# Optimization experiments

Hardware: AMD Instinct MI355X
Metric: run time of the kernel (lower is better)

The kernel has to match this reference:

```python
import jax, jax.numpy as jnp
import numpy as np

EPS = 1e-12  # F.normalize default eps (norm clamped to at least eps)


def setup_inputs() -> dict:
    key = jax.random.key(0)
    k1, k2, k3, k4 = jax.random.split(key, 4)
    B, Cin, Cout, H, W = 8, 128, 32, 256, 256
    x = jax.random.normal(k1, (B, Cin, H, W), dtype=jnp.float32)
    qk = jax.random.normal(k2, (B, 2 * Cout, H, W), dtype=jnp.float32)
    # 1x1 conv params (PyTorch Conv2d default init scale ~ 1/sqrt(fan_in))
    w_v = jax.random.normal(k3, (Cout, Cin), dtype=jnp.float32) / np.sqrt(Cin)
    b_v = jax.random.normal(k4, (Cout,), dtype=jnp.float32) / np.sqrt(Cin)
    temperature = jnp.ones((1, 1, 1), dtype=jnp.float32)
    return {"x": x, "qk": qk, "w_v": w_v, "b_v": b_v, "temperature": temperature}


def reference(x, qk, w_v, b_v, temperature):
    B, Cin, H, W = x.shape
    Co = w_v.shape[0]
    N = H * W
    # 1x1 conv == channel GEMM
    v = jnp.einsum('bchw,oc->bohw', x, w_v) + b_v[None, :, None, None]
    # split qk: k = first Co channels, q = last Co channels; head=1
    q = qk[:, Co:].reshape(B, 1, Co, N)
    k = qk[:, :Co].reshape(B, 1, Co, N)
    v = v.reshape(B, 1, Co, N)
    # L2-normalize over spatial dim (F.normalize: divide by max(norm, eps))
    q = q / jnp.maximum(jnp.linalg.norm(q, axis=-1, keepdims=True), EPS)
    k = k / jnp.maximum(jnp.linalg.norm(k, axis=-1, keepdims=True), EPS)
    # channel-wise (transposed) attention: [B,1,Co,Co]
    attn = jnp.einsum('bhcn,bhdn->bhcd', q, k) * temperature
    attn = jax.nn.softmax(attn, axis=-1)
    out = jnp.einsum('bhcd,bhdn->bhcn', attn, v)  # [B,1,Co,N]
    return out
```

## Files before the change

kernel.cpp:

```cpp
#include <hip/hip_runtime.h>
#include <hip/hip_bf16.h>
#include <math.h>

#define NB    8
#define CIN   128
#define CO    32
#define CH    64
#define NN    65536
#define CHUNKS 128
#define GXB   32
#define SPW   (NN/CHUNKS)
#define SLABS (SPW/16)

typedef __attribute__((ext_vector_type(8))) short bf16x8;
typedef __attribute__((ext_vector_type(16))) float f32x16;

__device__ __forceinline__ short f2bf(float f) {
    union { __hip_bfloat16 h; short s; } u;
    u.h = __float2bfloat16(f);
    return u.s;
}
__device__ __forceinline__ float bf2f(short s) {
    union { __hip_bfloat16 h; short s; } u;
    u.s = s;
    return __bfloat162float(u.h);
}

__global__ __launch_bounds__(256) void gram_kernel(const float* __restrict__ qk,
                                                   float* __restrict__ part,
                                                   float* __restrict__ partsq) {
    const int b = blockIdx.y;
    const int w = threadIdx.x >> 6;
    const int l = threadIdx.x & 63;
    const int chunk = blockIdx.x * 4 + w;
    const int c = l & 31;
    const int half = l >> 5;

    const float* qrow = qk + (size_t)b * CH * NN + (size_t)(CO + c) * NN
                        + (size_t)chunk * SPW + half * 8;
    const float* krow = qk + (size_t)b * CH * NN + (size_t)c * NN
                        + (size_t)chunk * SPW + half * 8;

    f32x16 acc = {};
    float sqq = 0.f, sqk = 0.f;

#pragma unroll 4
    for (int s = 0; s < SLABS; ++s) {
        float4 q0 = *(const float4*)(qrow + s * 16);
        float4 q1 = *(const float4*)(qrow + s * 16 + 4);
        float4 k0 = *(const float4*)(krow + s * 16);
        float4 k1 = *(const float4*)(krow + s * 16 + 4);

        float qf[8] = {q0.x, q0.y, q0.z, q0.w, q1.x, q1.y, q1.z, q1.w};
        float kf[8] = {k0.x, k0.y, k0.z, k0.w, k1.x, k1.y, k1.z, k1.w};

        bf16x8 ah, al, bh, bl;
#pragma unroll
        for (int j = 0; j < 8; ++j) {
            short hq = f2bf(qf[j]);
            ah[j] = hq;
            al[j] = f2bf(qf[j] - bf2f(hq));
            short hk = f2bf(kf[j]);
            bh[j] = hk;
            bl[j] = f2bf(kf[j] - bf2f(hk));
            sqq = fmaf(qf[j], qf[j], sqq);
            sqk = fmaf(kf[j], kf[j], sqk);
        }
        acc = __builtin_amdgcn_mfma_f32_32x32x16_bf16(ah, bh, acc, 0, 0, 0);
        acc = __builtin_amdgcn_mfma_f32_32x32x16_bf16(ah, bl, acc, 0, 0, 0);
        acc = __builtin_amdgcn_mfma_f32_32x32x16_bf16(al, bh, acc, 0, 0, 0);
    }

    sqq += __shfl_xor(sqq, 32);
    sqk += __shfl_xor(sqk, 32);
    if (half == 0) {
        float* psq = partsq + ((size_t)b * CHUNKS + chunk) * 64;
        psq[c] = sqk;
        psq[CO + c] = sqq;
    }

    float* pp = part + ((size_t)b * CHUNKS + chunk) * 1024;
#pragma unroll
    for (int r = 0; r < 16; ++r) {
        int row = (r & 3) + 8 * (r >> 2) + 4 * half;
        pp[row * 32 + c] = acc[r];
    }
}

__global__ __launch_bounds__(128) void reduce_kernel(const float* __restrict__ part,
                                                     const float* __restrict__ partsq,
                                                     float* __restrict__ Sred) {
    const int b = blockIdx.y;
    const int v = blockIdx.x * 64 + (threadIdx.x >> 1);
    const int h = threadIdx.x & 1;
    float s = 0.f;
    if (v < 1024) {
        const float* p = part + (size_t)b * CHUNKS * 1024 + v;
        for (int ch = h * (CHUNKS / 2); ch < (h + 1) * (CHUNKS / 2); ++ch)
            s += p[(size_t)ch * 1024];
    } else {
        const float* p = partsq + (size_t)b * CHUNKS * 64 + (v - 1024);
        for (int ch = h * (CHUNKS / 2); ch < (h + 1) * (CHUNKS / 2); ++ch)
            s += p[(size_t)ch * 64];
    }
    s += __shfl_xor(s, 1);
    if (h == 0) Sred[b * 1088 + v] = s;
}

__global__ __launch_bounds__(256) void attn_kernel(const float* __restrict__ Sred,
                                                   const float* __restrict__ w_v,
                                                   const float* __restrict__ b_v,
                                                   const float* __restrict__ temp,
                                                   float* __restrict__ Weff,
                                                   float* __restrict__ beff) {
    __shared__ float sS[1024];
    __shared__ float snorm[64];
    __shared__ float sA[1024];
    const int t = threadIdx.x;
    const int b = blockIdx.x;

    for (int i = t; i < 1024; i += 256) sS[i] = Sred[b * 1088 + i];
    if (t < 64) snorm[t] = fmaxf(sqrtf(Sred[b * 1088 + 1024 + t]), 1e-12f);
    __syncthreads();

    if (t < 32) {
        const float T = temp[0];
        const float qn = snorm[32 + t];
        float m = -1e30f;
        for (int d = 0; d < 32; ++d)
            m = fmaxf(m, sS[t * 32 + d] / (qn * snorm[d]) * T);
        float sum = 0.f;
        for (int d = 0; d < 32; ++d)
            sum += expf(sS[t * 32 + d] / (qn * snorm[d]) * T - m);
        const float inv = 1.f / sum;
        for (int d = 0; d < 32; ++d)
            sA[t * 32 + d] = expf(sS[t * 32 + d] / (qn * snorm[d]) * T - m) * inv;
    }
    __syncthreads();

    for (int idx = t; idx < CO * CIN; idx += 256) {
        int cc = idx >> 7;
        int ci = idx & 127;
        float s = 0.f;
#pragma unroll
        for (int d = 0; d < 32; ++d) s += sA[cc * 32 + d] * w_v[d * CIN + ci];
        Weff[(size_t)b * CO * CIN + idx] = s;
    }
    if (t < 32) {
        float s = 0.f;
#pragma unroll
        for (int d = 0; d < 32; ++d) s += sA[t * 32 + d] * b_v[d];
        beff[b * CO + t] = s;
    }
}

__global__ __launch_bounds__(256) void out_kernel(const float* __restrict__ x,
                                                  const float* __restrict__ Weff,
                                                  const float* __restrict__ beff,
                                                  float* __restrict__ out) {
    const int b = blockIdx.y;
    const int n0 = blockIdx.x * 512 + threadIdx.x * 2;
    const float* xb = x + (size_t)b * CIN * NN + n0;
    const float* Wb = Weff + (size_t)b * CO * CIN;
    const float* bb = beff + b * CO;

    float a0[CO], a1[CO];
#pragma unroll
    for (int o = 0; o < CO; ++o) { a0[o] = bb[o]; a1[o] = bb[o]; }

#pragma unroll 4
    for (int ci = 0; ci < CIN; ++ci) {
        float2 xv = *(const float2*)(xb + (size_t)ci * NN);
#pragma unroll
        for (int o = 0; o < CO; ++o) {
            float wv = Wb[o * CIN + ci];
            a0[o] = fmaf(wv, xv.x, a0[o]);
            a1[o] = fmaf(wv, xv.y, a1[o]);
        }
    }

    float* ob = out + (size_t)b * CO * NN + n0;
#pragma unroll
    for (int o = 0; o < CO; ++o) {
        float2 r;
        r.x = a0[o];
        r.y = a1[o];
        *(float2*)(ob + (size_t)o * NN) = r;
    }
}

extern "C" void kernel_launch(void* const* d_in, const int* in_sizes, int n_in,
                              void* d_out, int out_size, void* d_ws, size_t ws_size,
                              hipStream_t stream) {
    const float* x    = (const float*)d_in[0];
    const float* qk   = (const float*)d_in[1];
    const float* w_v  = (const float*)d_in[2];
    const float* b_v  = (const float*)d_in[3];
    const float* temp = (const float*)d_in[4];
    float* out = (float*)d_out;

    float* part   = (float*)d_ws;
    float* partsq = part + (size_t)NB * CHUNKS * 1024;
    float* Sred   = partsq + (size_t)NB * CHUNKS * 64;
    float* Weff   = Sred + (size_t)NB * 1088;
    float* beff   = Weff + (size_t)NB * CO * CIN;

    gram_kernel<<<dim3(GXB, NB), 256, 0, stream>>>(qk, part, partsq);
    reduce_kernel<<<dim3(17, NB), 128, 0, stream>>>(part, partsq, Sred);
    attn_kernel<<<dim3(NB), 256, 0, stream>>>(Sred, w_v, b_v, temp, Weff, beff);
    out_kernel<<<dim3(NN / 512, NB), 256, 0, stream>>>(x, Weff, beff, out);
}
```

Baseline: 119.9 us.

## Widen gram grid with in-block reduction, fuse reduce into finalize, vectorize weight loads

The gram kernel now launches 128 chunks per batch instead of 32. Each block's four waves split a chunk and sum their partial Gram matrices in shared memory before writing one result. The separate reduce kernel is folded into the attention/finalize kernel, which removes one launch but runs the 128-chunk reduction inside only 8 blocks. The output kernel reads the effective weights as float4 over four input channels, which cuts the number of scalar weight loads.

```diff
diff --git a/kernel.cpp b/kernel.cpp
--- a/kernel.cpp
+++ b/kernel.cpp
@@ -8,8 +8,8 @@
 #define CH    64
 #define NN    65536
 #define CHUNKS 128
-#define GXB   32
-#define SPW   (NN/CHUNKS)
+#define SPC   (NN/CHUNKS)
+#define SPW   (SPC/4)
 #define SLABS (SPW/16)
 
 typedef __attribute__((ext_vector_type(8))) short bf16x8;
@@ -29,22 +29,24 @@
 __global__ __launch_bounds__(256) void gram_kernel(const float* __restrict__ qk,
                                                    float* __restrict__ part,
                                                    float* __restrict__ partsq) {
+    __shared__ float red[4 * 1024];
+    __shared__ float red2[4 * 64];
+
     const int b = blockIdx.y;
+    const int chunk = blockIdx.x;
     const int w = threadIdx.x >> 6;
     const int l = threadIdx.x & 63;
-    const int chunk = blockIdx.x * 4 + w;
     const int c = l & 31;
     const int half = l >> 5;
 
-    const float* qrow = qk + (size_t)b * CH * NN + (size_t)(CO + c) * NN
-                        + (size_t)chunk * SPW + half * 8;
-    const float* krow = qk + (size_t)b * CH * NN + (size_t)c * NN
-                        + (size_t)chunk * SPW + half * 8;
+    const size_t colbase = (size_t)chunk * SPC + (size_t)w * SPW + half * 8;
+    const float* qrow = qk + (size_t)b * CH * NN + (size_t)(CO + c) * NN + colbase;
+    const float* krow = qk + (size_t)b * CH * NN + (size_t)c * NN + colbase;
 
     f32x16 acc = {};
     float sqq = 0.f, sqk = 0.f;
 
-#pragma unroll 4
+#pragma unroll 2
     for (int s = 0; s < SLABS; ++s) {
         float4 q0 = *(const float4*)(qrow + s * 16);
         float4 q1 = *(const float4*)(qrow + s * 16 + 4);
@@ -74,53 +76,59 @@
     sqq += __shfl_xor(sqq, 32);
     sqk += __shfl_xor(sqk, 32);
     if (half == 0) {
-        float* psq = partsq + ((size_t)b * CHUNKS + chunk) * 64;
-        psq[c] = sqk;
-        psq[CO + c] = sqq;
-    }
-
-    float* pp = part + ((size_t)b * CHUNKS + chunk) * 1024;
+        red2[w * 64 + c] = sqk;
+        red2[w * 64 + 32 + c] = sqq;
+    }
+
 #pragma unroll
     for (int r = 0; r < 16; ++r) {
         int row = (r & 3) + 8 * (r >> 2) + 4 * half;
-        pp[row * 32 + c] = acc[r];
-    }
-}
-
-__global__ __launch_bounds__(128) void reduce_kernel(const float* __restrict__ part,
-                                                     const float* __restrict__ partsq,
-                                                     float* __restrict__ Sred) {
-    const int b = blockIdx.y;
-    const int v = blockIdx.x * 64 + (threadIdx.x >> 1);
-    const int h = threadIdx.x & 1;
-    float s = 0.f;
-    if (v < 1024) {
-        const float* p = part + (size_t)b * CHUNKS * 1024 + v;
-        for (int ch = h * (CHUNKS / 2); ch < (h + 1) * (CHUNKS / 2); ++ch)
-            s += p[(size_t)ch * 1024];
-    } else {
-        const float* p = partsq + (size_t)b * CHUNKS * 64 + (v - 1024);
-        for (int ch = h * (CHUNKS / 2); ch < (h + 1) * (CHUNKS / 2); ++ch)
-            s += p[(size_t)ch * 64];
-    }
-    s += __shfl_xor(s, 1);
-    if (h == 0) Sred[b * 1088 + v] = s;
-}
-
-__global__ __launch_bounds__(256) void attn_kernel(const float* __restrict__ Sred,
-                                                   const float* __restrict__ w_v,
-                                                   const float* __restrict__ b_v,
-                                                   const float* __restrict__ temp,
-                                                   float* __restrict__ Weff,
-                                                   float* __restrict__ beff) {
+        red[w * 1024 + row * 32 + c] = acc[r];
+    }
+    __syncthreads();
+
+    float* pp = part + ((size_t)b * CHUNKS + chunk) * 1024;
+#pragma unroll
+    for (int k = 0; k < 4; ++k) {
+        int idx = threadIdx.x + k * 256;
+        pp[idx] = red[idx] + red[1024 + idx] + red[2048 + idx] + red[3072 + idx];
+    }
+    if (threadIdx.x < 64) {
+        partsq[((size_t)b * CHUNKS + chunk) * 64 + threadIdx.x] =
+            red2[threadIdx.x] + red2[64 + threadIdx.x] +
+            red2[128 + threadIdx.x] + red2[192 + threadIdx.x];
+    }
+}
+
+__global__ __launch_bounds__(256) void finalize_kernel(const float* __restrict__ part,
+                                                       const float* __restrict__ partsq,
+                                                       const float* __restrict__ w_v,
+                                                       const float* __restrict__ b_v,
+                                                       const float* __restrict__ temp,
+                                                       float* __restrict__ Weff,
+                                                       float* __restrict__ beff) {
     __shared__ float sS[1024];
     __shared__ float snorm[64];
     __shared__ float sA[1024];
     const int t = threadIdx.x;
     const int b = blockIdx.x;
 
-    for (int i = t; i < 1024; i += 256) sS[i] = Sred[b * 1088 + i];
-    if (t < 64) snorm[t] = fmaxf(sqrtf(Sred[b * 1088 + 1024 + t]), 1e-12f);
+    for (int v = t; v < 1024; v += 256) {
+        const float* p = part + (size_t)b * CHUNKS * 1024 + v;
+        float s = 0.f;
+#pragma unroll 16
+        for (int ch = 0; ch < CHUNKS; ++ch)
+            s += p[(size_t)ch * 1024];
+        sS[v] = s;
+    }
+    if (t < 64) {
+        const float* p = partsq + (size_t)b * CHUNKS * 64 + t;
+        float s = 0.f;
+#pragma unroll 16
+        for (int ch = 0; ch < CHUNKS; ++ch)
+            s += p[(size_t)ch * 64];
+        snorm[t] = fmaxf(sqrtf(s), 1e-12f);
+    }
     __syncthreads();
 
     if (t < 32) {
@@ -161,21 +169,29 @@
     const int b = blockIdx.y;
     const int n0 = blockIdx.x * 512 + threadIdx.x * 2;
     const float* xb = x + (size_t)b * CIN * NN + n0;
-    const float* Wb = Weff + (size_t)b * CO * CIN;
+    const float4* Wb4 = (const float4*)(Weff + (size_t)b * CO * CIN);
     const float* bb = beff + b * CO;
 
     float a0[CO], a1[CO];
 #pragma unroll
     for (int o = 0; o < CO; ++o) { a0[o] = bb[o]; a1[o] = bb[o]; }
 
-#pragma unroll 4
-    for (int ci = 0; ci < CIN; ++ci) {
-        float2 xv = *(const float2*)(xb + (size_t)ci * NN);
+    for (int ci4 = 0; ci4 < CIN / 4; ++ci4) {
+        float2 x0 = *(const float2*)(xb + (size_t)(ci4 * 4 + 0) * NN);
+        float2 x1 = *(const float2*)(xb + (size_t)(ci4 * 4 + 1) * NN);
+        float2 x2 = *(const float2*)(xb + (size_t)(ci4 * 4 + 2) * NN);
+        float2 x3 = *(const float2*)(xb + (size_t)(ci4 * 4 + 3) * NN);
 #pragma unroll
         for (int o = 0; o < CO; ++o) {
-            float wv = Wb[o * CIN + ci];
-            a0[o] = fmaf(wv, xv.x, a0[o]);
-            a1[o] = fmaf(wv, xv.y, a1[o]);
+            float4 w = Wb4[o * 32 + ci4];
+            a0[o] = fmaf(w.x, x0.x, a0[o]);
+            a1[o] = fmaf(w.x, x0.y, a1[o]);
+            a0[o] = fmaf(w.y, x1.x, a0[o]);
+            a1[o] = fmaf(w.y, x1.y, a1[o]);
+            a0[o] = fmaf(w.z, x2.x, a0[o]);
+            a1[o] = fmaf(w.z, x2.y, a1[o]);
+            a0[o] = fmaf(w.w, x3.x, a0[o]);
+            a1[o] = fmaf(w.w, x3.y, a1[o]);
         }
     }
 
@@ -201,12 +217,10 @@
 
     float* part   = (float*)d_ws;
     float* partsq = part + (size_t)NB * CHUNKS * 1024;
-    float* Sred   = partsq + (size_t)NB * CHUNKS * 64;
-    float* Weff   = Sred + (size_t)NB * 1088;
+    float* Weff   = partsq + (size_t)NB * CHUNKS * 64;
     float* beff   = Weff + (size_t)NB * CO * CIN;
 
-    gram_kernel<<<dim3(GXB, NB), 256, 0, stream>>>(qk, part, partsq);
-    reduce_kernel<<<dim3(17, NB), 128, 0, stream>>>(part, partsq, Sred);
-    attn_kernel<<<dim3(NB), 256, 0, stream>>>(Sred, w_v, b_v, temp, Weff, beff);
+    gram_kernel<<<dim3(CHUNKS, NB), 256, 0, stream>>>(qk, part, partsq);
+    finalize_kernel<<<dim3(NB), 256, 0, stream>>>(part, partsq, w_v, b_v, temp, Weff, beff);
     out_kernel<<<dim3(NN / 512, NB), 256, 0, stream>>>(x, Weff, beff, out);
 }
```

Result: slower. 135.0 us (+12.6%).

## Split gram chunks across eight waves with LDS reduction and upfront loads

Applied to the files above, without the earlier changes.

The gram kernel now uses one 512-thread block per chunk. Each of its eight waves handles one eighth of the chunk's columns. All of a wave's q/k loads are issued up front into registers to raise memory-level parallelism, and the eight wave-partial Gram matrices are summed in shared memory before one write per chunk. This gives 8x more waves in flight over the same data, which should better saturate HBM bandwidth, at the cost of 32KB LDS per block and a block-level sync plus reduction.

```diff
diff --git a/kernel.cpp b/kernel.cpp
--- a/kernel.cpp
+++ b/kernel.cpp
@@ -8,8 +8,9 @@
 #define CH    64
 #define NN    65536
 #define CHUNKS 128
-#define GXB   32
-#define SPW   (NN/CHUNKS)
+#define SPC   (NN/CHUNKS)
+#define WPB   8
+#define SPW   (SPC/WPB)
 #define SLABS (SPW/16)
 
 typedef __attribute__((ext_vector_type(8))) short bf16x8;
@@ -26,33 +27,42 @@
     return __bfloat162float(u.h);
 }
 
-__global__ __launch_bounds__(256) void gram_kernel(const float* __restrict__ qk,
+__global__ __launch_bounds__(512) void gram_kernel(const float* __restrict__ qk,
                                                    float* __restrict__ part,
                                                    float* __restrict__ partsq) {
+    __shared__ float red[WPB * 1024];
+    __shared__ float red2[WPB * 64];
+
     const int b = blockIdx.y;
-    const int w = threadIdx.x >> 6;
-    const int l = threadIdx.x & 63;
-    const int chunk = blockIdx.x * 4 + w;
+    const int chunk = blockIdx.x;
+    const int t = threadIdx.x;
+    const int w = t >> 6;
+    const int l = t & 63;
     const int c = l & 31;
     const int half = l >> 5;
 
-    const float* qrow = qk + (size_t)b * CH * NN + (size_t)(CO + c) * NN
-                        + (size_t)chunk * SPW + half * 8;
-    const float* krow = qk + (size_t)b * CH * NN + (size_t)c * NN
-                        + (size_t)chunk * SPW + half * 8;
+    const size_t colbase = (size_t)chunk * SPC + (size_t)w * SPW + half * 8;
+    const float* qrow = qk + (size_t)b * CH * NN + (size_t)(CO + c) * NN + colbase;
+    const float* krow = qk + (size_t)b * CH * NN + (size_t)c * NN + colbase;
+
+    float4 qA[SLABS][2], kA[SLABS][2];
+#pragma unroll
+    for (int s = 0; s < SLABS; ++s) {
+        qA[s][0] = *(const float4*)(qrow + s * 16);
+        qA[s][1] = *(const float4*)(qrow + s * 16 + 4);
+        kA[s][0] = *(const float4*)(krow + s * 16);
+        kA[s][1] = *(const float4*)(krow + s * 16 + 4);
+    }
 
     f32x16 acc = {};
     float sqq = 0.f, sqk = 0.f;
 
-#pragma unroll 4
+#pragma unroll
     for (int s = 0; s < SLABS; ++s) {
-        float4 q0 = *(const float4*)(qrow + s * 16);
-        float4 q1 = *(const float4*)(qrow + s * 16 + 4);
-        float4 k0 = *(const float4*)(krow + s * 16);
-        float4 k1 = *(const float4*)(krow + s * 16 + 4);
-
-        float qf[8] = {q0.x, q0.y, q0.z, q0.w, q1.x, q1.y, q1.z, q1.w};
-        float kf[8] = {k0.x, k0.y, k0.z, k0.w, k1.x, k1.y, k1.z, k1.w};
+        float qf[8] = {qA[s][0].x, qA[s][0].y, qA[s][0].z, qA[s][0].w,
+                       qA[s][1].x, qA[s][1].y, qA[s][1].z, qA[s][1].w};
+        float kf[8] = {kA[s][0].x, kA[s][0].y, kA[s][0].z, kA[s][0].w,
+                       kA[s][1].x, kA[s][1].y, kA[s][1].z, kA[s][1].w};
 
         bf16x8 ah, al, bh, bl;
 #pragma unroll
@@ -74,16 +84,31 @@
     sqq += __shfl_xor(sqq, 32);
     sqk += __shfl_xor(sqk, 32);
     if (half == 0) {
-        float* psq = partsq + ((size_t)b * CHUNKS + chunk) * 64;
-        psq[c] = sqk;
-        psq[CO + c] = sqq;
-    }
-
-    float* pp = part + ((size_t)b * CHUNKS + chunk) * 1024;
+        red2[w * 64 + c] = sqk;
+        red2[w * 64 + 32 + c] = sqq;
+    }
+
 #pragma unroll
     for (int r = 0; r < 16; ++r) {
         int row = (r & 3) + 8 * (r >> 2) + 4 * half;
-        pp[row * 32 + c] = acc[r];
+        red[w * 1024 + row * 32 + c] = acc[r];
+    }
+    __syncthreads();
+
+    float* pp = part + ((size_t)b * CHUNKS + chunk) * 1024;
+#pragma unroll
+    for (int k = 0; k < 2; ++k) {
+        int idx = t + k * 512;
+        float s = 0.f;
+#pragma unroll
+        for (int ww = 0; ww < WPB; ++ww) s += red[ww * 1024 + idx];
+        pp[idx] = s;
+    }
+    if (t < 64) {
+        float s = 0.f;
+#pragma unroll
+        for (int ww = 0; ww < WPB; ++ww) s += red2[ww * 64 + t];
+        partsq[((size_t)b * CHUNKS + chunk) * 64 + t] = s;
     }
 }
 
@@ -205,7 +230,7 @@
     float* Weff   = Sred + (size_t)NB * 1088;
     float* beff   = Weff + (size_t)NB * CO * CIN;
 
-    gram_kernel<<<dim3(GXB, NB), 256, 0, stream>>>(qk, part, partsq);
+    gram_kernel<<<dim3(CHUNKS, NB), 512, 0, stream>>>(qk, part, partsq);
     reduce_kernel<<<dim3(17, NB), 128, 0, stream>>>(part, partsq, Sred);
     attn_kernel<<<dim3(NB), 256, 0, stream>>>(Sred, w_v, b_v, temp, Weff, beff);
     out_kernel<<<dim3(NN / 512, NB), 256, 0, stream>>>(x, Weff, beff, out);
```

Measured after the change: 126.0 us. 1.05x slower.

## Stage qk tiles through swizzled LDS with coalesced loads in gram kernel

Applied to the files above, without the earlier changes.

The gram kernel now loads 64x128 column tiles of qk into shared memory with fully coalesced float4 loads, using an XOR swizzle to avoid bank conflicts. It also computes the squared norms during the load. The MFMA bf16 split-precision products then read their operands from LDS. The four waves' partial Gram matrices are reduced in shared memory before being written, so each block emits one partial instead of four. This cuts partial-sum traffic and reduce-kernel work, but adds block-wide syncs and shared-memory round trips per tile.

```diff
diff --git a/kernel.cpp b/kernel.cpp
--- a/kernel.cpp
+++ b/kernel.cpp
@@ -7,10 +7,10 @@
 #define CO    32
 #define CH    64
 #define NN    65536
-#define CHUNKS 128
-#define GXB   32
-#define SPW   (NN/CHUNKS)
-#define SLABS (SPW/16)
+#define CPB   1024
+#define GBLK  (NN/CPB)
+#define TCOLS 128
+#define NTILES (CPB/TCOLS)
 
 typedef __attribute__((ext_vector_type(8))) short bf16x8;
 typedef __attribute__((ext_vector_type(16))) float f32x16;
@@ -29,61 +29,92 @@
 __global__ __launch_bounds__(256) void gram_kernel(const float* __restrict__ qk,
                                                    float* __restrict__ part,
                                                    float* __restrict__ partsq) {
+    __shared__ float smem[CH * TCOLS];
+    float4* tile4 = (float4*)smem;
+
     const int b = blockIdx.y;
-    const int w = threadIdx.x >> 6;
-    const int l = threadIdx.x & 63;
-    const int chunk = blockIdx.x * 4 + w;
+    const int blk = blockIdx.x;
+    const int t = threadIdx.x;
+    const int w = t >> 6;
+    const int l = t & 63;
     const int c = l & 31;
     const int half = l >> 5;
 
-    const float* qrow = qk + (size_t)b * CH * NN + (size_t)(CO + c) * NN
-                        + (size_t)chunk * SPW + half * 8;
-    const float* krow = qk + (size_t)b * CH * NN + (size_t)c * NN
-                        + (size_t)chunk * SPW + half * 8;
+    const float* qkb = qk + (size_t)b * CH * NN;
+    const size_t colbase0 = (size_t)blk * CPB;
 
     f32x16 acc = {};
-    float sqq = 0.f, sqk = 0.f;
-
-#pragma unroll 4
-    for (int s = 0; s < SLABS; ++s) {
-        float4 q0 = *(const float4*)(qrow + s * 16);
-        float4 q1 = *(const float4*)(qrow + s * 16 + 4);
-        float4 k0 = *(const float4*)(krow + s * 16);
-        float4 k1 = *(const float4*)(krow + s * 16 + 4);
-
-        float qf[8] = {q0.x, q0.y, q0.z, q0.w, q1.x, q1.y, q1.z, q1.w};
-        float kf[8] = {k0.x, k0.y, k0.z, k0.w, k1.x, k1.y, k1.z, k1.w};
-
-        bf16x8 ah, al, bh, bl;
-#pragma unroll
-        for (int j = 0; j < 8; ++j) {
-            short hq = f2bf(qf[j]);
-            ah[j] = hq;
-            al[j] = f2bf(qf[j] - bf2f(hq));
-            short hk = f2bf(kf[j]);
-            bh[j] = hk;
-            bl[j] = f2bf(kf[j] - bf2f(hk));
-            sqq = fmaf(qf[j], qf[j], sqq);
-            sqk = fmaf(kf[j], kf[j], sqk);
+    float sq[8] = {0.f, 0.f, 0.f, 0.f, 0.f, 0.f, 0.f, 0.f};
+
+    for (int tau = 0; tau < NTILES; ++tau) {
+        const size_t colbase = colbase0 + (size_t)tau * TCOLS;
+        __syncthreads();
+#pragma unroll
+        for (int k = 0; k < 8; ++k) {
+            int flat = t + k * 256;
+            int row = flat >> 5;
+            int col4 = flat & 31;
+            float4 v = *(const float4*)(qkb + (size_t)row * NN + colbase + col4 * 4);
+            sq[k] = fmaf(v.x, v.x, sq[k]);
+            sq[k] = fmaf(v.y, v.y, sq[k]);
+            sq[k] = fmaf(v.z, v.z, sq[k]);
+            sq[k] = fmaf(v.w, v.w, sq[k]);
+            tile4[row * 32 + (col4 ^ (row & 7))] = v;
         }
-        acc = __builtin_amdgcn_mfma_f32_32x32x16_bf16(ah, bh, acc, 0, 0, 0);
-        acc = __builtin_amdgcn_mfma_f32_32x32x16_bf16(ah, bl, acc, 0, 0, 0);
-        acc = __builtin_amdgcn_mfma_f32_32x32x16_bf16(al, bh, acc, 0, 0, 0);
-    }
-
-    sqq += __shfl_xor(sqq, 32);
-    sqk += __shfl_xor(sqk, 32);
-    if (half == 0) {
-        float* psq = partsq + ((size_t)b * CHUNKS + chunk) * 64;
-        psq[c] = sqk;
-        psq[CO + c] = sqq;
-    }
-
-    float* pp = part + ((size_t)b * CHUNKS + chunk) * 1024;
+        __syncthreads();
+#pragma unroll
+        for (int ss = 0; ss < 2; ++ss) {
+            const int s = 2 * w + ss;
+            const int f0 = s * 4 + half * 2;
+            const int qrow = CO + c;
+            const int krow = c;
+            const int sw = c & 7;
+            float4 q0 = tile4[qrow * 32 + (f0 ^ sw)];
+            float4 q1 = tile4[qrow * 32 + ((f0 + 1) ^ sw)];
+            float4 k0 = tile4[krow * 32 + (f0 ^ sw)];
+            float4 k1 = tile4[krow * 32 + ((f0 + 1) ^ sw)];
+
+            float qf[8] = {q0.x, q0.y, q0.z, q0.w, q1.x, q1.y, q1.z, q1.w};
+            float kf[8] = {k0.x, k0.y, k0.z, k0.w, k1.x, k1.y, k1.z, k1.w};
+
+            bf16x8 ah, al, bh, bl;
+#pragma unroll
+            for (int j = 0; j < 8; ++j) {
+                short hq = f2bf(qf[j]);
+                ah[j] = hq;
+                al[j] = f2bf(qf[j] - bf2f(hq));
+                short hk = f2bf(kf[j]);
+                bh[j] = hk;
+                bl[j] = f2bf(kf[j] - bf2f(hk));
+            }
+            acc = __builtin_amdgcn_mfma_f32_32x32x16_bf16(ah, bh, acc, 0, 0, 0);
+            acc = __builtin_amdgcn_mfma_f32_32x32x16_bf16(ah, bl, acc, 0, 0, 0);
+            acc = __builtin_amdgcn_mfma_f32_32x32x16_bf16(al, bh, acc, 0, 0, 0);
+        }
+    }
+    __syncthreads();
+
 #pragma unroll
     for (int r = 0; r < 16; ++r) {
         int row = (r & 3) + 8 * (r >> 2) + 4 * half;
-        pp[row * 32 + c] = acc[r];
+        smem[w * 1024 + row * 32 + c] = acc[r];
+    }
+#pragma unroll
+    for (int k = 0; k < 8; ++k)
+        smem[4096 + ((t >> 5) + 8 * k) * 32 + (t & 31)] = sq[k];
+    __syncthreads();
+
+    float* pp = part + ((size_t)b * GBLK + blk) * 1024;
+#pragma unroll
+    for (int j = 0; j < 4; ++j) {
+        int idx = t + j * 256;
+        pp[idx] = smem[idx] + smem[1024 + idx] + smem[2048 + idx] + smem[3072 + idx];
+    }
+    if (t < 64) {
+        float s = 0.f;
+#pragma unroll
+        for (int i = 0; i < 32; ++i) s += smem[4096 + t * 32 + i];
+        partsq[((size_t)b * GBLK + blk) * 64 + t] = s;
     }
 }
 
@@ -95,12 +126,12 @@
     const int h = threadIdx.x & 1;
     float s = 0.f;
     if (v < 1024) {
-        const float* p = part + (size_t)b * CHUNKS * 1024 + v;
-        for (int ch = h * (CHUNKS / 2); ch < (h + 1) * (CHUNKS / 2); ++ch)
+        const float* p = part + (size_t)b * GBLK * 1024 + v;
+        for (int ch = h * (GBLK / 2); ch < (h + 1) * (GBLK / 2); ++ch)
             s += p[(size_t)ch * 1024];
     } else {
-        const float* p = partsq + (size_t)b * CHUNKS * 64 + (v - 1024);
-        for (int ch = h * (CHUNKS / 2); ch < (h + 1) * (CHUNKS / 2); ++ch)
+        const float* p = partsq + (size_t)b * GBLK * 64 + (v - 1024);
+        for (int ch = h * (GBLK / 2); ch < (h + 1) * (GBLK / 2); ++ch)
             s += p[(size_t)ch * 64];
     }
     s += __shfl_xor(s, 1);
@@ -200,12 +231,12 @@
     float* out = (float*)d_out;
 
     float* part   = (float*)d_ws;
-    float* partsq = part + (size_t)NB * CHUNKS * 1024;
-    float* Sred   = partsq + (size_t)NB * CHUNKS * 64;
+    float* partsq = part + (size_t)NB * GBLK * 1024;
+    float* Sred   = partsq + (size_t)NB * GBLK * 64;
     float* Weff   = Sred + (size_t)NB * 1088;
     float* beff   = Weff + (size_t)NB * CO * CIN;
 
-    gram_kernel<<<dim3(GXB, NB), 256, 0, stream>>>(qk, part, partsq);
+    gram_kernel<<<dim3(GBLK, NB), 256, 0, stream>>>(qk, part, partsq);
     reduce_kernel<<<dim3(17, NB), 128, 0, stream>>>(part, partsq, Sred);
     attn_kernel<<<dim3(NB), 256, 0, stream>>>(Sred, w_v, b_v, temp, Weff, beff);
     out_kernel<<<dim3(NN / 512, NB), 256, 0, stream>>>(x, Weff, beff, out);
```

After: 121.3 us. No clear change (+1.2%).
